# Optimization experiments

Hardware: AMD Instinct MI355X
Metric: run time of the kernel (lower is better)

## Reference

```python
import jax, jax.numpy as jnp
import numpy as np

B, T, C, H = 8, 2048, 1024, 64  # batch, seq_len, num_embed, size_head


def setup_inputs() -> dict:
    key = jax.random.key(0)
    kx, kq, kk, kv = jax.random.split(key, 4)
    return {
        "x": jax.random.normal(kx, (B, T, C), dtype=jnp.float32),
        "Wq": jax.random.normal(kq, (C, H), dtype=jnp.float32) * 0.02,
        "Wk": jax.random.normal(kk, (C, H), dtype=jnp.float32) * 0.02,
        "Wv": jax.random.normal(kv, (C, H), dtype=jnp.float32) * 0.02,
    }


def reference(x, Wq, Wk, Wv):
    # x: [B, T, C]; single-head causal self-attention.
    # NOTE: original scales by num_channels = x.shape[-1] (= C), not head dim.
    num_channels = x.shape[-1]
    q = jnp.einsum("btc,ch->bth", x, Wq)
    k = jnp.einsum("btc,ch->bth", x, Wk)
    v = jnp.einsum("btc,ch->bth", x, Wv)
    w = jnp.einsum("bqh,bkh->bqk", q, k) * (num_channels ** -0.5)  # [B,T,T]
    causal = jnp.tril(jnp.ones((x.shape[1], x.shape[1]), dtype=bool))
    w = jnp.where(causal, w, -jnp.inf)
    w = jax.nn.softmax(w, axis=-1)
    # dropout is identity in eval/reference mode
    out = jnp.einsum("bqk,bkh->bqh", w, v)  # [B,T,H]
    return out
```

## Files before the change

### kernel.cpp

```cpp
#include <hip/hip_runtime.h>
#include <hip/hip_bf16.h>
#include <stdint.h>

#define Bn 8
#define Tn 2048
#define Cn 1024
#define Hn 64

typedef __attribute__((ext_vector_type(8))) short bf16x8;
typedef __attribute__((ext_vector_type(4))) short bf16x4;
typedef __attribute__((ext_vector_type(4))) float f32x4;

#if defined(__HIP_DEVICE_COMPILE__) && !__has_builtin(__builtin_amdgcn_mfma_f32_16x16x16bf16_1k)
#error "mfma_f32_16x16x16bf16_1k required on gfx950"
#endif
#define MFMA16(a, b, c) __builtin_amdgcn_mfma_f32_16x16x16bf16_1k(a, b, c, 0, 0, 0)
#define MFMA32(a, b, c) __builtin_amdgcn_mfma_f32_16x16x32_bf16(a, b, c, 0, 0, 0)

__device__ __forceinline__ unsigned short f2bf(float f) {
  union { float f; unsigned int u; } v; v.f = f;
  unsigned int u = v.u;
  u = u + 0x7fffu + ((u >> 16) & 1u);
  return (unsigned short)(u >> 16);
}

__device__ __forceinline__ void gload16(const unsigned short* g, unsigned short* l) {
  __builtin_amdgcn_global_load_lds(
      (const __attribute__((address_space(1))) unsigned int*)(const void*)g,
      (__attribute__((address_space(3))) unsigned int*)(void*)l, 16, 0, 0);
}

__global__ __launch_bounds__(256) void k_prep(const float* __restrict__ Wq,
                                              const float* __restrict__ Wk,
                                              const float* __restrict__ Wv,
                                              unsigned short* __restrict__ Wt) {
  const int m = blockIdx.x >> 6;
  const int h = blockIdx.x & 63;
  const float* W = (m == 0) ? Wq : (m == 1) ? Wk : Wv;
  const int tid = threadIdx.x;
  unsigned short* dst = Wt + ((size_t)(m * 64 + h)) * 1024;
#pragma unroll
  for (int j = 0; j < 4; ++j) {
    int c = j * 256 + tid;
    dst[c] = f2bf(W[(size_t)c * 64 + h]);
  }
}

__global__ __launch_bounds__(256, 2) void k_qkv(const float* __restrict__ x,
                                                const unsigned short* __restrict__ Wt,
                                                unsigned short* __restrict__ Q,
                                                unsigned short* __restrict__ K,
                                                unsigned short* __restrict__ Vt) {
  __shared__ __align__(16) char smem[32256];
  unsigned short (*xs)[72] = (unsigned short (*)[72])smem;
  unsigned short (*wsh)[72] = (unsigned short (*)[72])(smem + 32 * 72 * 2);
  unsigned short (*os)[200] = (unsigned short (*)[200])smem;

  const int tid = threadIdx.x;
  const int lane = tid & 63;
  const int wid = tid >> 6;
  const int wm = wid >> 1, wn = wid & 1;
  const int l15 = lane & 15, g = lane >> 4;
  const int r0 = blockIdx.x * 32;

  f32x4 acc[6];
#pragma unroll
  for (int j = 0; j < 6; ++j)
#pragma unroll
    for (int r = 0; r < 4; ++r) acc[j][r] = 0.f;

  const int srow = tid >> 3;
  const int scol = (tid & 7) * 8;

  for (int kt = 0; kt < 16; ++kt) {
    const int k0 = kt * 64;
    const float* xp = x + (size_t)(r0 + srow) * 1024 + k0 + scol;
    {
      float4 v0 = *(const float4*)xp;
      float4 v1 = *(const float4*)(xp + 4);
      ushort4 b0, b1;
      b0.x = f2bf(v0.x); b0.y = f2bf(v0.y); b0.z = f2bf(v0.z); b0.w = f2bf(v0.w);
      b1.x = f2bf(v1.x); b1.y = f2bf(v1.y); b1.z = f2bf(v1.z); b1.w = f2bf(v1.w);
      *(ushort4*)&xs[srow][scol] = b0;
      *(ushort4*)&xs[srow][scol + 4] = b1;
    }
#pragma unroll
    for (int j = 0; j < 6; ++j) {
      int u = j * 256 + tid;
      int row = u >> 3, ch = u & 7;
      uint4 w = *(const uint4*)(Wt + (size_t)row * 1024 + k0 + ch * 8);
      *(uint4*)&wsh[row][ch * 8] = w;
    }
    __syncthreads();
#pragma unroll
    for (int kf = 0; kf < 2; ++kf) {
      bf16x8 a = *(const bf16x8*)&xs[wm * 16 + l15][kf * 32 + g * 8];
#pragma unroll
      for (int nf = 0; nf < 6; ++nf) {
        bf16x8 bfr = *(const bf16x8*)&wsh[wn * 96 + nf * 16 + l15][kf * 32 + g * 8];
        acc[nf] = MFMA32(a, bfr, acc[nf]);
      }
    }
    __syncthreads();
  }

#pragma unroll
  for (int nf = 0; nf < 6; ++nf)
#pragma unroll
    for (int r = 0; r < 4; ++r)
      os[wm * 16 + 4 * g + r][wn * 96 + nf * 16 + l15] = f2bf(acc[nf][r]);
  __syncthreads();

  const int b = r0 >> 11;
  const int t0 = r0 & 2047;
  {
    int row = tid >> 3, ch = tid & 7;
    *(uint4*)(Q + (size_t)(r0 + row) * 64 + ch * 8) = *(const uint4*)&os[row][ch * 8];
    *(uint4*)(K + (size_t)(r0 + row) * 64 + ch * 8) = *(const uint4*)&os[row][64 + ch * 8];
  }
  {
    int h = tid >> 2, tc = (tid & 3) * 8;
    unsigned short tmp[8];
#pragma unroll
    for (int r = 0; r < 8; ++r) tmp[r] = os[tc + r][128 + h];
    *(uint4*)(Vt + ((size_t)b * 64 + h) * 2048 + t0 + tc) = *(const uint4*)tmp;
  }
}

__global__ __launch_bounds__(256, 2) void k_attn_coop(const unsigned short* __restrict__ Q,
                                                      const unsigned short* __restrict__ K,
                                                      const unsigned short* __restrict__ Vt,
                                                      float* __restrict__ out,
                                                      float* __restrict__ po,
                                                      float* __restrict__ pml) {
  __shared__ __align__(16) unsigned short lds[2][8192];

  const int tid = threadIdx.x;
  const int lane = tid & 63;
  const int l15 = lane & 15, g = lane >> 4;
  const int wid = __builtin_amdgcn_readfirstlane(tid >> 6);

  const int bi = blockIdx.x;
  const int b = bi / 144;
  const int id = bi - b * 144;
  int gq = 0;
#pragma unroll
  for (int t = 1; t < 8; ++t)
    if (id >= 2 * t * (t + 1)) gq = t;
  const int rem = id - 2 * gq * (gq + 1);
  const int ql = rem / (gq + 1);
  const int s = rem - ql * (gq + 1);
  const int qt = 4 * gq + ql;
  const int qblk = qt * 64;
  const int klo = 256 * s;
  const int khi = min(klo + 256, qblk + 64);
  const int nt = (khi - klo + 63) >> 6;
  const int q0w = qblk + wid * 16;

  const unsigned short* Qb = Q + (size_t)b * Tn * Hn;
  const unsigned short* Kb = K + (size_t)b * Tn * Hn;
  const unsigned short* Vb = Vt + (size_t)b * Hn * Tn;

  bf16x8 bq0 = *(const bf16x8*)(Qb + (size_t)(q0w + l15) * 64 + g * 8);
  bf16x8 bq1 = *(const bf16x8*)(Qb + (size_t)(q0w + l15) * 64 + 32 + g * 8);

  f32x4 o[4];
#pragma unroll
  for (int hf = 0; hf < 4; ++hf)
#pragma unroll
    for (int r = 0; r < 4; ++r) o[hf][r] = 0.f;
  float m = -1e30f, lsum = 0.f;
  const float sc = 0.03125f * 1.44269504088896f;

  auto stage = [&](int buf, int k0) {
    unsigned short* tb = &lds[buf][0];
#pragma unroll
    for (int j = 0; j < 4; ++j) {
      const int p = wid * 256 + j * 64 + lane;
      const unsigned short* src;
      if (wid < 2) {
        const int row = p >> 3, c = p & 7;
        src = Kb + (size_t)(k0 + row) * 64 + ((c ^ (row & 7)) * 8);
      } else {
        const int q = p - 512;
        const int h = q >> 3, c = q & 7;
        src = Vb + (size_t)h * Tn + k0 + ((c ^ (h & 7)) * 8);
      }
      gload16(src, tb + wid * 2048 + j * 512);
    }
  };

  stage(0, klo);
  __syncthreads();

  for (int t = 0; t < nt; ++t) {
    const int cur = t & 1;
    const int k0 = klo + t * 64;
    if (t + 1 < nt) stage(cur ^ 1, klo + (t + 1) * 64);

    const unsigned short* kt = &lds[cur][0];
    const unsigned short* vt = &lds[cur][4096];

    f32x4 sacc[4];
#pragma unroll
    for (int kc = 0; kc < 4; ++kc) {
      const int row = kc * 16 + l15;
      const int sw = row & 7;
      bf16x8 ka = *(const bf16x8*)&kt[row * 64 + ((g ^ sw) * 8)];
      bf16x8 kb2 = *(const bf16x8*)&kt[row * 64 + (((4 + g) ^ sw) * 8)];
#pragma unroll
      for (int r = 0; r < 4; ++r) sacc[kc][r] = 0.f;
      sacc[kc] = MFMA32(ka, bq0, sacc[kc]);
      sacc[kc] = MFMA32(kb2, bq1, sacc[kc]);
    }
    float sv[4][4];
    if (k0 + 63 > q0w) {
      const int q = q0w + l15;
#pragma unroll
      for (int kc = 0; kc < 4; ++kc)
#pragma unroll
        for (int r = 0; r < 4; ++r) {
          int key = k0 + kc * 16 + 4 * g + r;
          sv[kc][r] = (key <= q) ? sacc[kc][r] * sc : -1e30f;
        }
    } else {
#pragma unroll
      for (int kc = 0; kc < 4; ++kc)
#pragma unroll
        for (int r = 0; r < 4; ++r) sv[kc][r] = sacc[kc][r] * sc;
    }
    float pm = sv[0][0];
#pragma unroll
    for (int kc = 0; kc < 4; ++kc)
#pragma unroll
      for (int r = 0; r < 4; ++r) pm = fmaxf(pm, sv[kc][r]);
    if (__any(pm > m + 8.f)) {
      pm = fmaxf(pm, __shfl_xor(pm, 16));
      pm = fmaxf(pm, __shfl_xor(pm, 32));
      float mn = fmaxf(m, pm);
      float alpha = exp2f(m - mn);
      lsum *= alpha;
      float an[4];
#pragma unroll
      for (int r = 0; r < 4; ++r) an[r] = __shfl(alpha, 4 * g + r);
#pragma unroll
      for (int hf = 0; hf < 4; ++hf)
#pragma unroll
        for (int r = 0; r < 4; ++r) o[hf][r] *= an[r];
      m = mn;
    }
    float ts = 0.f;
#pragma unroll
    for (int kc = 0; kc < 4; ++kc)
#pragma unroll
      for (int r = 0; r < 4; ++r) { sv[kc][r] = exp2f(sv[kc][r] - m); ts += sv[kc][r]; }
    ts += __shfl_xor(ts, 16);
    ts += __shfl_xor(ts, 32);
    lsum += ts;
    bf16x4 pa[4];
#pragma unroll
    for (int kc = 0; kc < 4; ++kc) {
      pa[kc][0] = (short)f2bf(sv[kc][0]); pa[kc][1] = (short)f2bf(sv[kc][1]);
      pa[kc][2] = (short)f2bf(sv[kc][2]); pa[kc][3] = (short)f2bf(sv[kc][3]);
    }
    bf16x4 vf[4][4];
#pragma unroll
    for (int hf = 0; hf < 4; ++hf) {
      const int h = hf * 16 + l15, hs = h & 7;
#pragma unroll
      for (int kc = 0; kc < 4; ++kc) {
        const int gran = (kc * 2 + (g >> 1)) ^ hs;
        vf[hf][kc] = *(const bf16x4*)&vt[h * 64 + gran * 8 + (g & 1) * 4];
      }
    }
#pragma unroll
    for (int hf = 0; hf < 4; ++hf)
#pragma unroll
      for (int kc = 0; kc < 4; ++kc)
        o[hf] = MFMA16(pa[kc], vf[hf][kc], o[hf]);

    __syncthreads();
  }

  if (qt >= 4) {
    const int slot = b * 140 + id - 4;
    float* pob = po + (size_t)slot * 4096;
#pragma unroll
    for (int hf = 0; hf < 4; ++hf)
#pragma unroll
      for (int r = 0; r < 4; ++r)
        pob[(16 * wid + 4 * g + r) * 64 + hf * 16 + l15] = o[hf][r];
    if (lane < 16) {
      pml[(size_t)slot * 128 + 16 * wid + l15] = m;
      pml[(size_t)slot * 128 + 64 + 16 * wid + l15] = lsum;
    }
  } else {
    const float il = 1.f / lsum;
    float iln[4];
#pragma unroll
    for (int r = 0; r < 4; ++r) iln[r] = __shfl(il, 4 * g + r);
    float* ob = out + ((size_t)b * Tn + q0w) * 64;
#pragma unroll
    for (int hf = 0; hf < 4; ++hf)
#pragma unroll
      for (int r = 0; r < 4; ++r)
        ob[(size_t)(4 * g + r) * 64 + hf * 16 + l15] = o[hf][r] * iln[r];
  }
}

__global__ __launch_bounds__(256) void k_comb(const float* __restrict__ po,
                                              const float* __restrict__ pml,
                                              float* __restrict__ out) {
  const int qt = 4 + blockIdx.x;
  const int b = blockIdx.y;
  const int gq = qt >> 2, ql = qt & 3;
  const int nseg = gq + 1;
  const int base = b * 140 + 2 * gq * (gq + 1) + ql * (gq + 1) - 4;
  const int r = threadIdx.x >> 2;
  const int cg = threadIdx.x & 3;

  float mv[8], lv[8], M = -1e30f;
#pragma unroll
  for (int s = 0; s < 8; ++s)
    if (s < nseg) {
      mv[s] = pml[(size_t)(base + s) * 128 + r];
      lv[s] = pml[(size_t)(base + s) * 128 + 64 + r];
      M = fmaxf(M, mv[s]);
    }
  float w[8], L = 0.f;
#pragma unroll
  for (int s = 0; s < 8; ++s)
    if (s < nseg) { w[s] = exp2f(mv[s] - M); L += w[s] * lv[s]; }

  float acc[16];
#pragma unroll
  for (int c = 0; c < 16; ++c) acc[c] = 0.f;
#pragma unroll
  for (int s = 0; s < 8; ++s)
    if (s < nseg) {
      const float* pb = po + (size_t)(base + s) * 4096 + r * 64 + cg * 16;
#pragma unroll
      for (int j = 0; j < 4; ++j) {
        float4 v = *(const float4*)(pb + 4 * j);
        acc[4 * j + 0] += w[s] * v.x; acc[4 * j + 1] += w[s] * v.y;
        acc[4 * j + 2] += w[s] * v.z; acc[4 * j + 3] += w[s] * v.w;
      }
    }
  const float invL = 1.f / L;
  float* ob = out + ((size_t)b * Tn + qt * 64 + r) * 64 + cg * 16;
#pragma unroll
  for (int j = 0; j < 4; ++j) {
    float4 v;
    v.x = acc[4 * j + 0] * invL; v.y = acc[4 * j + 1] * invL;
    v.z = acc[4 * j + 2] * invL; v.w = acc[4 * j + 3] * invL;
    *(float4*)(ob + 4 * j) = v;
  }
}

__global__ __launch_bounds__(256, 2) void k_attn_wave(const unsigned short* __restrict__ Q,
                                                      const unsigned short* __restrict__ K,
                                                      const unsigned short* __restrict__ Vt,
                                                      float* __restrict__ out) {
  const int tid = threadIdx.x;
  const int lane = tid & 63;
  const int l15 = lane & 15, g = lane >> 4;
  const int wid = tid >> 6;
  const int task = blockIdx.x * 4 + wid;
  const int b = task >> 7, qt = task & 127;
  const int q0 = qt * 16;
  const int nt = (q0 + 16 + 63) >> 6;

  const unsigned short* Qb = Q + (size_t)b * Tn * Hn;
  const unsigned short* Kb = K + (size_t)b * Tn * Hn;
  const unsigned short* Vb = Vt + (size_t)b * Hn * Tn;

  bf16x8 bq0 = *(const bf16x8*)(Qb + (size_t)(q0 + l15) * 64 + g * 8);
  bf16x8 bq1 = *(const bf16x8*)(Qb + (size_t)(q0 + l15) * 64 + 32 + g * 8);

  f32x4 o[4];
#pragma unroll
  for (int hf = 0; hf < 4; ++hf)
#pragma unroll
    for (int r = 0; r < 4; ++r) o[hf][r] = 0.f;
  float m = -1e30f, lsum = 0.f;
  const float sc = 0.03125f * 1.44269504088896f;

  for (int t = 0; t < nt; ++t) {
    const int k0 = t * 64;
    bf16x4 vf[4][4];
#pragma unroll
    for (int hf = 0; hf < 4; ++hf) {
      const unsigned short* vrow = Vb + (size_t)(hf * 16 + l15) * Tn + k0 + 4 * g;
#pragma unroll
      for (int kc = 0; kc < 4; ++kc) vf[hf][kc] = *(const bf16x4*)(vrow + kc * 16);
    }
    f32x4 sacc[4];
#pragma unroll
    for (int kc = 0; kc < 4; ++kc) {
      const unsigned short* kp = Kb + (size_t)(k0 + kc * 16 + l15) * 64 + g * 8;
      bf16x8 ka = *(const bf16x8*)kp;
      bf16x8 kb2 = *(const bf16x8*)(kp + 32);
#pragma unroll
      for (int r = 0; r < 4; ++r) sacc[kc][r] = 0.f;
      sacc[kc] = MFMA32(ka, bq0, sacc[kc]);
      sacc[kc] = MFMA32(kb2, bq1, sacc[kc]);
    }
    float sv[4][4];
    if (k0 + 63 > q0) {
      const int q = q0 + l15;
#pragma unroll
      for (int kc = 0; kc < 4; ++kc)
#pragma unroll
        for (int r = 0; r < 4; ++r) {
          int key = k0 + kc * 16 + 4 * g + r;
          sv[kc][r] = (key <= q) ? sacc[kc][r] * sc : -1e30f;
        }
    } else {
#pragma unroll
      for (int kc = 0; kc < 4; ++kc)
#pragma unroll
        for (int r = 0; r < 4; ++r) sv[kc][r] = sacc[kc][r] * sc;
    }
    float pm = sv[0][0];
#pragma unroll
    for (int kc = 0; kc < 4; ++kc)
#pragma unroll
      for (int r = 0; r < 4; ++r) pm = fmaxf(pm, sv[kc][r]);
    if (__any(pm > m + 8.f)) {
      pm = fmaxf(pm, __shfl_xor(pm, 16));
      pm = fmaxf(pm, __shfl_xor(pm, 32));
      float mn = fmaxf(m, pm);
      float alpha = exp2f(m - mn);
      lsum *= alpha;
      float an[4];
#pragma unroll
      for (int r = 0; r < 4; ++r) an[r] = __shfl(alpha, 4 * g + r);
#pragma unroll
      for (int hf = 0; hf < 4; ++hf)
#pragma unroll
        for (int r = 0; r < 4; ++r) o[hf][r] *= an[r];
      m = mn;
    }
    float ts = 0.f;
#pragma unroll
    for (int kc = 0; kc < 4; ++kc)
#pragma unroll
      for (int r = 0; r < 4; ++r) { sv[kc][r] = exp2f(sv[kc][r] - m); ts += sv[kc][r]; }
    ts += __shfl_xor(ts, 16);
    ts += __shfl_xor(ts, 32);
    lsum += ts;
    bf16x4 pa[4];
#pragma unroll
    for (int kc = 0; kc < 4; ++kc) {
      pa[kc][0] = (short)f2bf(sv[kc][0]); pa[kc][1] = (short)f2bf(sv[kc][1]);
      pa[kc][2] = (short)f2bf(sv[kc][2]); pa[kc][3] = (short)f2bf(sv[kc][3]);
    }
#pragma unroll
    for (int hf = 0; hf < 4; ++hf)
#pragma unroll
      for (int kc = 0; kc < 4; ++kc)
        o[hf] = MFMA16(pa[kc], vf[hf][kc], o[hf]);
  }
  const float il = 1.f / lsum;
  float iln[4];
#pragma unroll
  for (int r = 0; r < 4; ++r) iln[r] = __shfl(il, 4 * g + r);
  float* ob = out + ((size_t)b * Tn + q0) * 64;
#pragma unroll
  for (int hf = 0; hf < 4; ++hf)
#pragma unroll
    for (int r = 0; r < 4; ++r)
      ob[(size_t)(4 * g + r) * 64 + hf * 16 + l15] = o[hf][r] * iln[r];
}

extern "C" void kernel_launch(void* const* d_in, const int* in_sizes, int n_in,
                              void* d_out, int out_size, void* d_ws, size_t ws_size,
                              hipStream_t stream) {
  const float* x  = (const float*)d_in[0];
  const float* Wq = (const float*)d_in[1];
  const float* Wk = (const float*)d_in[2];
  const float* Wv = (const float*)d_in[3];
  float* out = (float*)d_out;

  unsigned short* Wt = (unsigned short*)d_ws;
  unsigned short* Qs = Wt + 3 * 64 * 1024;
  unsigned short* Ks = Qs + (size_t)Bn * Tn * Hn;
  unsigned short* Vt = Ks + (size_t)Bn * Tn * Hn;
  const size_t bf_bytes = (3 * 64 * 1024 + 3 * (size_t)Bn * Tn * Hn) * 2;
  float* po = (float*)((char*)d_ws + bf_bytes);

  const size_t nslots = (size_t)Bn * 140;
  float* pml = po + nslots * 4096;
  const size_t need = bf_bytes + nslots * (4096 + 128) * sizeof(float);

  hipLaunchKernelGGL(k_prep, dim3(192), dim3(256), 0, stream, Wq, Wk, Wv, Wt);
  hipLaunchKernelGGL(k_qkv, dim3(512), dim3(256), 0, stream, x, Wt, Qs, Ks, Vt);
  if (ws_size >= need) {
    hipLaunchKernelGGL(k_attn_coop, dim3(1152), dim3(256), 0, stream, Qs, Ks, Vt, out, po, pml);
    hipLaunchKernelGGL(k_comb, dim3(28, 8), dim3(256), 0, stream, po, pml, out);
  } else {
    hipLaunchKernelGGL(k_attn_wave, dim3(256), dim3(256), 0, stream, Qs, Ks, Vt, out);
  }
}
```

Measured before the change: 55.26 us.

## Double-buffer QKV projection LDS tiles and remap attention block order

```diff
diff --git a/kernel.cpp b/kernel.cpp
--- a/kernel.cpp
+++ b/kernel.cpp
@@ -51,10 +51,7 @@
                                                 unsigned short* __restrict__ Q,
                                                 unsigned short* __restrict__ K,
                                                 unsigned short* __restrict__ Vt) {
-  __shared__ __align__(16) char smem[32256];
-  unsigned short (*xs)[72] = (unsigned short (*)[72])smem;
-  unsigned short (*wsh)[72] = (unsigned short (*)[72])(smem + 32 * 72 * 2);
-  unsigned short (*os)[200] = (unsigned short (*)[200])smem;
+  __shared__ __align__(16) char smem[64512];
 
   const int tid = threadIdx.x;
   const int lane = tid & 63;
@@ -62,36 +59,50 @@
   const int wm = wid >> 1, wn = wid & 1;
   const int l15 = lane & 15, g = lane >> 4;
   const int r0 = blockIdx.x * 32;
-
-  f32x4 acc[6];
-#pragma unroll
-  for (int j = 0; j < 6; ++j)
-#pragma unroll
-    for (int r = 0; r < 4; ++r) acc[j][r] = 0.f;
-
   const int srow = tid >> 3;
   const int scol = (tid & 7) * 8;
 
-  for (int kt = 0; kt < 16; ++kt) {
-    const int k0 = kt * 64;
-    const float* xp = x + (size_t)(r0 + srow) * 1024 + k0 + scol;
-    {
-      float4 v0 = *(const float4*)xp;
-      float4 v1 = *(const float4*)(xp + 4);
-      ushort4 b0, b1;
-      b0.x = f2bf(v0.x); b0.y = f2bf(v0.y); b0.z = f2bf(v0.z); b0.w = f2bf(v0.w);
-      b1.x = f2bf(v1.x); b1.y = f2bf(v1.y); b1.z = f2bf(v1.z); b1.w = f2bf(v1.w);
-      *(ushort4*)&xs[srow][scol] = b0;
-      *(ushort4*)&xs[srow][scol + 4] = b1;
-    }
+  f32x4 acc[6];
+#pragma unroll
+  for (int j = 0; j < 6; ++j)
+#pragma unroll
+    for (int r = 0; r < 4; ++r) acc[j][r] = 0.f;
+
+  float4 xv0, xv1;
+  uint4 wv[6];
+  auto gload = [&](int kt) {
+    const float* xp = x + (size_t)(r0 + srow) * 1024 + kt * 64 + scol;
+    xv0 = *(const float4*)xp;
+    xv1 = *(const float4*)(xp + 4);
 #pragma unroll
     for (int j = 0; j < 6; ++j) {
       int u = j * 256 + tid;
-      int row = u >> 3, ch = u & 7;
-      uint4 w = *(const uint4*)(Wt + (size_t)row * 1024 + k0 + ch * 8);
-      *(uint4*)&wsh[row][ch * 8] = w;
-    }
+      wv[j] = *(const uint4*)(Wt + (size_t)(u >> 3) * 1024 + kt * 64 + (u & 7) * 8);
+    }
+  };
+  auto swrite = [&](int bb) {
+    unsigned short (*xs)[72] = (unsigned short (*)[72])(smem + bb * 32256);
+    unsigned short (*wsh)[72] = (unsigned short (*)[72])(smem + bb * 32256 + 32 * 72 * 2);
+    ushort4 b0, b1;
+    b0.x = f2bf(xv0.x); b0.y = f2bf(xv0.y); b0.z = f2bf(xv0.z); b0.w = f2bf(xv0.w);
+    b1.x = f2bf(xv1.x); b1.y = f2bf(xv1.y); b1.z = f2bf(xv1.z); b1.w = f2bf(xv1.w);
+    *(ushort4*)&xs[srow][scol] = b0;
+    *(ushort4*)&xs[srow][scol + 4] = b1;
+#pragma unroll
+    for (int j = 0; j < 6; ++j) {
+      int u = j * 256 + tid;
+      *(uint4*)&wsh[u >> 3][(u & 7) * 8] = wv[j];
+    }
+  };
+
+  gload(0);
+  swrite(0);
+  for (int kt = 0; kt < 16; ++kt) {
+    const int cur = kt & 1;
+    if (kt < 15) gload(kt + 1);
     __syncthreads();
+    unsigned short (*xs)[72] = (unsigned short (*)[72])(smem + cur * 32256);
+    unsigned short (*wsh)[72] = (unsigned short (*)[72])(smem + cur * 32256 + 32 * 72 * 2);
 #pragma unroll
     for (int kf = 0; kf < 2; ++kf) {
       bf16x8 a = *(const bf16x8*)&xs[wm * 16 + l15][kf * 32 + g * 8];
@@ -101,9 +112,11 @@
         acc[nf] = MFMA32(a, bfr, acc[nf]);
       }
     }
-    __syncthreads();
-  }
-
+    if (kt < 15) swrite(cur ^ 1);
+  }
+
+  unsigned short (*os)[200] = (unsigned short (*)[200])smem;
+  __syncthreads();
 #pragma unroll
   for (int nf = 0; nf < 6; ++nf)
 #pragma unroll
@@ -127,7 +140,7 @@
   }
 }
 
-__global__ __launch_bounds__(256, 2) void k_attn_coop(const unsigned short* __restrict__ Q,
+__global__ __launch_bounds__(256, 3) void k_attn_coop(const unsigned short* __restrict__ Q,
                                                       const unsigned short* __restrict__ K,
                                                       const unsigned short* __restrict__ Vt,
                                                       float* __restrict__ out,
@@ -140,7 +153,8 @@
   const int l15 = lane & 15, g = lane >> 4;
   const int wid = __builtin_amdgcn_readfirstlane(tid >> 6);
 
-  const int bi = blockIdx.x;
+  const int raw = blockIdx.x;
+  const int bi = (raw & 7) * 144 + (raw >> 3);
   const int b = bi / 144;
   const int id = bi - b * 144;
   int gq = 0;
```

After: 91.10 us. 64.9% more time.

## Double-buffer QKV projection with async global-to-LDS loads and swizzled tiles

Applied to the files above, without the earlier changes.

```diff
diff --git a/kernel.cpp b/kernel.cpp
--- a/kernel.cpp
+++ b/kernel.cpp
@@ -24,10 +24,10 @@
   return (unsigned short)(u >> 16);
 }
 
-__device__ __forceinline__ void gload16(const unsigned short* g, unsigned short* l) {
+__device__ __forceinline__ void gload16(const void* g, void* l) {
   __builtin_amdgcn_global_load_lds(
-      (const __attribute__((address_space(1))) unsigned int*)(const void*)g,
-      (__attribute__((address_space(3))) unsigned int*)(void*)l, 16, 0, 0);
+      (const __attribute__((address_space(1))) unsigned int*)g,
+      (__attribute__((address_space(3))) unsigned int*)l, 16, 0, 0);
 }
 
 __global__ __launch_bounds__(256) void k_prep(const float* __restrict__ Wq,
@@ -46,80 +46,95 @@
   }
 }
 
-__global__ __launch_bounds__(256, 2) void k_qkv(const float* __restrict__ x,
+__global__ __launch_bounds__(256, 1) void k_qkv(const float* __restrict__ x,
                                                 const unsigned short* __restrict__ Wt,
                                                 unsigned short* __restrict__ Q,
                                                 unsigned short* __restrict__ K,
                                                 unsigned short* __restrict__ Vt) {
-  __shared__ __align__(16) char smem[32256];
-  unsigned short (*xs)[72] = (unsigned short (*)[72])smem;
-  unsigned short (*wsh)[72] = (unsigned short (*)[72])(smem + 32 * 72 * 2);
-  unsigned short (*os)[200] = (unsigned short (*)[200])smem;
+  __shared__ __align__(16) char smem[81920];
 
   const int tid = threadIdx.x;
   const int lane = tid & 63;
-  const int wid = tid >> 6;
-  const int wm = wid >> 1, wn = wid & 1;
+  const int wid = __builtin_amdgcn_readfirstlane(tid >> 6);
   const int l15 = lane & 15, g = lane >> 4;
-  const int r0 = blockIdx.x * 32;
-
-  f32x4 acc[6];
-#pragma unroll
-  for (int j = 0; j < 6; ++j)
+  const int r0 = blockIdx.x * 64;
+
+  f32x4 acc[12];
+#pragma unroll
+  for (int j = 0; j < 12; ++j)
 #pragma unroll
     for (int r = 0; r < 4; ++r) acc[j][r] = 0.f;
 
-  const int srow = tid >> 3;
-  const int scol = (tid & 7) * 8;
-
+  auto stage = [&](int buf, int kt) {
+    char* base = smem + buf * 40960;
+    const int k0 = kt * 64;
+#pragma unroll
+    for (int j = 0; j < 4; ++j) {
+      const int c = wid * 4 + j;
+      const int row = c * 4 + (lane >> 4);
+      const int lg = (lane & 15) ^ (row & 7);
+      gload16(x + (size_t)(r0 + row) * 1024 + k0 + lg * 4,
+              base + c * 1024);
+    }
+#pragma unroll
+    for (int j = 0; j < 6; ++j) {
+      const int c = j * 4 + wid;
+      const int row = c * 8 + (lane >> 3);
+      const int lg = (lane & 7) ^ (row & 7);
+      gload16(Wt + (size_t)row * 1024 + k0 + lg * 8,
+              base + 16384 + c * 1024);
+    }
+  };
+
+  stage(0, 0);
+  const int myrow = wid * 16 + l15;
+  const int rs = myrow & 7;
   for (int kt = 0; kt < 16; ++kt) {
-    const int k0 = kt * 64;
-    const float* xp = x + (size_t)(r0 + srow) * 1024 + k0 + scol;
-    {
-      float4 v0 = *(const float4*)xp;
-      float4 v1 = *(const float4*)(xp + 4);
-      ushort4 b0, b1;
-      b0.x = f2bf(v0.x); b0.y = f2bf(v0.y); b0.z = f2bf(v0.z); b0.w = f2bf(v0.w);
-      b1.x = f2bf(v1.x); b1.y = f2bf(v1.y); b1.z = f2bf(v1.z); b1.w = f2bf(v1.w);
-      *(ushort4*)&xs[srow][scol] = b0;
-      *(ushort4*)&xs[srow][scol + 4] = b1;
-    }
-#pragma unroll
-    for (int j = 0; j < 6; ++j) {
-      int u = j * 256 + tid;
-      int row = u >> 3, ch = u & 7;
-      uint4 w = *(const uint4*)(Wt + (size_t)row * 1024 + k0 + ch * 8);
-      *(uint4*)&wsh[row][ch * 8] = w;
-    }
+    const int cur = kt & 1;
     __syncthreads();
+    if (kt < 15) stage(cur ^ 1, kt + 1);
+    const char* base = smem + cur * 40960;
+    const float* xf = (const float*)base;
+    const unsigned short* wf = (const unsigned short*)(base + 16384);
 #pragma unroll
     for (int kf = 0; kf < 2; ++kf) {
-      bf16x8 a = *(const bf16x8*)&xs[wm * 16 + l15][kf * 32 + g * 8];
-#pragma unroll
-      for (int nf = 0; nf < 6; ++nf) {
-        bf16x8 bfr = *(const bf16x8*)&wsh[wn * 96 + nf * 16 + l15][kf * 32 + g * 8];
-        acc[nf] = MFMA32(a, bfr, acc[nf]);
+      f32x4 x0 = *(const f32x4*)&xf[myrow * 64 + (((kf * 8 + 2 * g) ^ rs) * 4)];
+      f32x4 x1 = *(const f32x4*)&xf[myrow * 64 + (((kf * 8 + 2 * g + 1) ^ rs) * 4)];
+      bf16x8 a;
+      a[0] = (short)f2bf(x0[0]); a[1] = (short)f2bf(x0[1]);
+      a[2] = (short)f2bf(x0[2]); a[3] = (short)f2bf(x0[3]);
+      a[4] = (short)f2bf(x1[0]); a[5] = (short)f2bf(x1[1]);
+      a[6] = (short)f2bf(x1[2]); a[7] = (short)f2bf(x1[3]);
+#pragma unroll
+      for (int nf = 0; nf < 12; ++nf) {
+        const int row = nf * 16 + l15;
+        bf16x8 b = *(const bf16x8*)&wf[row * 64 + (((kf * 4 + g) ^ (row & 7)) * 8)];
+        acc[nf] = MFMA32(a, b, acc[nf]);
       }
     }
-    __syncthreads();
-  }
-
-#pragma unroll
-  for (int nf = 0; nf < 6; ++nf)
+  }
+
+  unsigned short (*os)[200] = (unsigned short (*)[200])smem;
+#pragma unroll
+  for (int nf = 0; nf < 12; ++nf)
 #pragma unroll
     for (int r = 0; r < 4; ++r)
-      os[wm * 16 + 4 * g + r][wn * 96 + nf * 16 + l15] = f2bf(acc[nf][r]);
+      os[wid * 16 + 4 * g + r][nf * 16 + l15] = f2bf(acc[nf][r]);
   __syncthreads();
 
   const int b = r0 >> 11;
   const int t0 = r0 & 2047;
-  {
-    int row = tid >> 3, ch = tid & 7;
+#pragma unroll
+  for (int j = 0; j < 2; ++j) {
+    int u = j * 256 + tid;
+    int row = u >> 3, ch = u & 7;
     *(uint4*)(Q + (size_t)(r0 + row) * 64 + ch * 8) = *(const uint4*)&os[row][ch * 8];
     *(uint4*)(K + (size_t)(r0 + row) * 64 + ch * 8) = *(const uint4*)&os[row][64 + ch * 8];
   }
-  {
-    int h = tid >> 2, tc = (tid & 3) * 8;
+#pragma unroll
+  for (int j = 0; j < 2; ++j) {
+    int u = j * 256 + tid;
+    int h = u >> 3, tc = (u & 7) * 8;
     unsigned short tmp[8];
 #pragma unroll
     for (int r = 0; r < 8; ++r) tmp[r] = os[tc + r][128 + h];
@@ -127,7 +142,7 @@
   }
 }
 
-__global__ __launch_bounds__(256, 2) void k_attn_coop(const unsigned short* __restrict__ Q,
+__global__ __launch_bounds__(256, 3) void k_attn_coop(const unsigned short* __restrict__ Q,
                                                       const unsigned short* __restrict__ K,
                                                       const unsigned short* __restrict__ Vt,
                                                       float* __restrict__ out,
@@ -140,7 +155,8 @@
   const int l15 = lane & 15, g = lane >> 4;
   const int wid = __builtin_amdgcn_readfirstlane(tid >> 6);
 
-  const int bi = blockIdx.x;
+  const int raw = blockIdx.x;
+  const int bi = (raw & 7) * 144 + (raw >> 3);
   const int b = bi / 144;
   const int id = bi - b * 144;
   int gq = 0;
@@ -494,7 +510,7 @@
   const size_t need = bf_bytes + nslots * (4096 + 128) * sizeof(float);
 
   hipLaunchKernelGGL(k_prep, dim3(192), dim3(256), 0, stream, Wq, Wk, Wv, Wt);
-  hipLaunchKernelGGL(k_qkv, dim3(512), dim3(256), 0, stream, x, Wt, Qs, Ks, Vt);
+  hipLaunchKernelGGL(k_qkv, dim3(256), dim3(256), 0, stream, x, Wt, Qs, Ks, Vt);
   if (ws_size >= need) {
     hipLaunchKernelGGL(k_attn_coop, dim3(1152), dim3(256), 0, stream, Qs, Ks, Vt, out, po, pml);
     hipLaunchKernelGGL(k_comb, dim3(28, 8), dim3(256), 0, stream, po, pml, out);
```

After: 54.26 us. Within noise of the previous version (-1.8%).

## Halve QKV projection row tile, raise occupancy, remap attention block order

Applied to the files above, without the earlier changes.

```diff
diff --git a/kernel.cpp b/kernel.cpp
--- a/kernel.cpp
+++ b/kernel.cpp
@@ -24,10 +24,10 @@
   return (unsigned short)(u >> 16);
 }
 
-__device__ __forceinline__ void gload16(const unsigned short* g, unsigned short* l) {
+__device__ __forceinline__ void gload16(const void* g, void* l) {
   __builtin_amdgcn_global_load_lds(
-      (const __attribute__((address_space(1))) unsigned int*)(const void*)g,
-      (__attribute__((address_space(3))) unsigned int*)(void*)l, 16, 0, 0);
+      (const __attribute__((address_space(1))) unsigned int*)g,
+      (__attribute__((address_space(3))) unsigned int*)l, 16, 0, 0);
 }
 
 __global__ __launch_bounds__(256) void k_prep(const float* __restrict__ Wq,
@@ -46,43 +46,38 @@
   }
 }
 
-__global__ __launch_bounds__(256, 2) void k_qkv(const float* __restrict__ x,
+__global__ __launch_bounds__(256, 4) void k_qkv(const float* __restrict__ x,
                                                 const unsigned short* __restrict__ Wt,
                                                 unsigned short* __restrict__ Q,
                                                 unsigned short* __restrict__ K,
                                                 unsigned short* __restrict__ Vt) {
-  __shared__ __align__(16) char smem[32256];
+  __shared__ __align__(16) char smem[29952];
   unsigned short (*xs)[72] = (unsigned short (*)[72])smem;
-  unsigned short (*wsh)[72] = (unsigned short (*)[72])(smem + 32 * 72 * 2);
+  unsigned short (*wsh)[72] = (unsigned short (*)[72])(smem + 2304);
   unsigned short (*os)[200] = (unsigned short (*)[200])smem;
 
   const int tid = threadIdx.x;
   const int lane = tid & 63;
   const int wid = tid >> 6;
-  const int wm = wid >> 1, wn = wid & 1;
   const int l15 = lane & 15, g = lane >> 4;
-  const int r0 = blockIdx.x * 32;
-
-  f32x4 acc[6];
-#pragma unroll
-  for (int j = 0; j < 6; ++j)
+  const int r0 = blockIdx.x * 16;
+
+  f32x4 acc[3];
+#pragma unroll
+  for (int j = 0; j < 3; ++j)
 #pragma unroll
     for (int r = 0; r < 4; ++r) acc[j][r] = 0.f;
 
-  const int srow = tid >> 3;
-  const int scol = (tid & 7) * 8;
+  const int xrow = tid >> 4;
+  const int xc = (tid & 15) * 4;
 
   for (int kt = 0; kt < 16; ++kt) {
     const int k0 = kt * 64;
-    const float* xp = x + (size_t)(r0 + srow) * 1024 + k0 + scol;
     {
-      float4 v0 = *(const float4*)xp;
-      float4 v1 = *(const float4*)(xp + 4);
-      ushort4 b0, b1;
-      b0.x = f2bf(v0.x); b0.y = f2bf(v0.y); b0.z = f2bf(v0.z); b0.w = f2bf(v0.w);
-      b1.x = f2bf(v1.x); b1.y = f2bf(v1.y); b1.z = f2bf(v1.z); b1.w = f2bf(v1.w);
-      *(ushort4*)&xs[srow][scol] = b0;
-      *(ushort4*)&xs[srow][scol + 4] = b1;
+      float4 v = *(const float4*)(x + (size_t)(r0 + xrow) * 1024 + k0 + xc);
+      ushort4 bv;
+      bv.x = f2bf(v.x); bv.y = f2bf(v.y); bv.z = f2bf(v.z); bv.w = f2bf(v.w);
+      *(ushort4*)&xs[xrow][xc] = bv;
     }
 #pragma unroll
     for (int j = 0; j < 6; ++j) {
@@ -94,10 +89,10 @@
     __syncthreads();
 #pragma unroll
     for (int kf = 0; kf < 2; ++kf) {
-      bf16x8 a = *(const bf16x8*)&xs[wm * 16 + l15][kf * 32 + g * 8];
-#pragma unroll
-      for (int nf = 0; nf < 6; ++nf) {
-        bf16x8 bfr = *(const bf16x8*)&wsh[wn * 96 + nf * 16 + l15][kf * 32 + g * 8];
+      bf16x8 a = *(const bf16x8*)&xs[l15][kf * 32 + g * 8];
+#pragma unroll
+      for (int nf = 0; nf < 3; ++nf) {
+        bf16x8 bfr = *(const bf16x8*)&wsh[wid * 48 + nf * 16 + l15][kf * 32 + g * 8];
         acc[nf] = MFMA32(a, bfr, acc[nf]);
       }
     }
@@ -105,29 +100,32 @@
   }
 
 #pragma unroll
-  for (int nf = 0; nf < 6; ++nf)
+  for (int nf = 0; nf < 3; ++nf)
 #pragma unroll
     for (int r = 0; r < 4; ++r)
-      os[wm * 16 + 4 * g + r][wn * 96 + nf * 16 + l15] = f2bf(acc[nf][r]);
+      os[4 * g + r][wid * 48 + nf * 16 + l15] = f2bf(acc[nf][r]);
   __syncthreads();
 
   const int b = r0 >> 11;
   const int t0 = r0 & 2047;
   {
-    int row = tid >> 3, ch = tid & 7;
-    *(uint4*)(Q + (size_t)(r0 + row) * 64 + ch * 8) = *(const uint4*)&os[row][ch * 8];
-    *(uint4*)(K + (size_t)(r0 + row) * 64 + ch * 8) = *(const uint4*)&os[row][64 + ch * 8];
+    int u = tid & 127;
+    int row = u >> 3, ch = u & 7;
+    if (tid < 128)
+      *(uint4*)(Q + (size_t)(r0 + row) * 64 + ch * 8) = *(const uint4*)&os[row][ch * 8];
+    else
+      *(uint4*)(K + (size_t)(r0 + row) * 64 + ch * 8) = *(const uint4*)&os[row][64 + ch * 8];
   }
   {
-    int h = tid >> 2, tc = (tid & 3) * 8;
-    unsigned short tmp[8];
-#pragma unroll
-    for (int r = 0; r < 8; ++r) tmp[r] = os[tc + r][128 + h];
-    *(uint4*)(Vt + ((size_t)b * 64 + h) * 2048 + t0 + tc) = *(const uint4*)tmp;
-  }
-}
-
-__global__ __launch_bounds__(256, 2) void k_attn_coop(const unsigned short* __restrict__ Q,
+    int h = tid >> 2, qd = tid & 3;
+    unsigned short tmp[4];
+#pragma unroll
+    for (int r = 0; r < 4; ++r) tmp[r] = os[qd * 4 + r][128 + h];
+    *(ushort4*)(Vt + ((size_t)b * 64 + h) * 2048 + t0 + qd * 4) = *(const ushort4*)tmp;
+  }
+}
+
+__global__ __launch_bounds__(256, 3) void k_attn_coop(const unsigned short* __restrict__ Q,
                                                       const unsigned short* __restrict__ K,
                                                       const unsigned short* __restrict__ Vt,
                                                       float* __restrict__ out,
@@ -140,7 +138,8 @@
   const int l15 = lane & 15, g = lane >> 4;
   const int wid = __builtin_amdgcn_readfirstlane(tid >> 6);
 
-  const int bi = blockIdx.x;
+  const int raw = blockIdx.x;
+  const int bi = (raw & 7) * 144 + (raw >> 3);
   const int b = bi / 144;
   const int id = bi - b * 144;
   int gq = 0;
@@ -494,7 +493,7 @@
   const size_t need = bf_bytes + nslots * (4096 + 128) * sizeof(float);
 
   hipLaunchKernelGGL(k_prep, dim3(192), dim3(256), 0, stream, Wq, Wk, Wv, Wt);
-  hipLaunchKernelGGL(k_qkv, dim3(512), dim3(256), 0, stream, x, Wt, Qs, Ks, Vt);
+  hipLaunchKernelGGL(k_qkv, dim3(1024), dim3(256), 0, stream, x, Wt, Qs, Ks, Vt);
   if (ws_size >= need) {
     hipLaunchKernelGGL(k_attn_coop, dim3(1152), dim3(256), 0, stream, Qs, Ks, Vt, out, po, pml);
     hipLaunchKernelGGL(k_comb, dim3(28, 8), dim3(256), 0, stream, po, pml, out);
```

Measured after the change: 60.44 us. 9.4% more time.
